# Kernel optimization log

Hardware: AMD Instinct MI355X
Metric: run time of the kernel (lower is better)

The kernel has to match this reference:

```python
import jax, jax.numpy as jnp
import numpy as np

HEADS = 16
DIM_HEAD = 64


def setup_inputs() -> dict:
    key = jax.random.key(0)
    k1, k2, k3 = jax.random.split(key, 3)
    b, n, dim = 4, 2048, 1024
    inner = HEADS * DIM_HEAD  # 1024
    x = jax.random.normal(k1, (b, n, dim), dtype=jnp.float32)
    # Dense weights, scaled like Glorot-ish init to keep softmax well-behaved
    w_qkv = jax.random.normal(k2, (dim, 3 * inner), dtype=jnp.float32) * (dim ** -0.5)
    w_out = jax.random.normal(k3, (inner, dim), dtype=jnp.float32) * (inner ** -0.5)
    b_out = jnp.zeros((dim,), dtype=jnp.float32)
    return {"x": x, "w_qkv": w_qkv, "w_out": w_out, "b_out": b_out}


def reference(x, w_qkv, w_out, b_out):
    b, n, dim = x.shape
    scale = DIM_HEAD ** -0.5
    qkv = x @ w_qkv  # [b, n, 3*h*d]
    q, k, v = jnp.split(qkv, 3, axis=-1)
    # 'b n (h d) -> b h n d'
    split_heads = lambda t: t.reshape(b, n, HEADS, DIM_HEAD).transpose(0, 2, 1, 3)
    q, k, v = split_heads(q), split_heads(k), split_heads(v)
    sim = jnp.einsum('bhid,bhjd->bhij', q, k) * scale  # [b, h, n, n]
    attn = jax.nn.softmax(sim, axis=-1)
    out = jnp.einsum('bhij,bhjd->bhid', attn, v)  # [b, h, n, d]
    out = out.transpose(0, 2, 1, 3).reshape(b, n, HEADS * DIM_HEAD)
    return out @ w_out + b_out  # dropout rate 0.0 -> identity
```

## Files before the change

### kernel.cpp

```cpp
#include <hip/hip_runtime.h>
#include <cstdint>

#define HEADS 16
#define DH 64
#define SEQ 2048
#define BATCH 4
#define DIM 1024
#define MTOT (BATCH*SEQ)
#define NQKV (3*DIM)

typedef short bf16x8 __attribute__((ext_vector_type(8)));
typedef float f32x4 __attribute__((ext_vector_type(4)));
typedef float f32x16 __attribute__((ext_vector_type(16)));

__device__ __forceinline__ unsigned short f2bf(float f) {
  union { float fv; unsigned int u; } c; c.fv = f;
  unsigned int u = c.u;
  u += 0x7FFFu + ((u >> 16) & 1u);
  return (unsigned short)(u >> 16);
}

__device__ __forceinline__ unsigned int cvtpk(float lo, float hi) {
  unsigned int r;
  asm("v_cvt_pk_bf16_f32 %0, %1, %2" : "=v"(r) : "v"(lo), "v"(hi));
  return r;
}

__device__ __forceinline__ f32x4 mfma16(bf16x8 a, bf16x8 b, f32x4 c) {
  return __builtin_amdgcn_mfma_f32_16x16x32_bf16(a, b, c, 0, 0, 0);
}
__device__ __forceinline__ f32x16 mfma32(bf16x8 a, bf16x8 b, f32x16 c) {
  return __builtin_amdgcn_mfma_f32_32x32x16_bf16(a, b, c, 0, 0, 0);
}

typedef const __attribute__((address_space(1))) unsigned int* gas_ptr;
typedef __attribute__((address_space(3))) unsigned int* las_ptr;
__device__ __forceinline__ void gl2lds16(const void* g, void* l) {
  __builtin_amdgcn_global_load_lds((gas_ptr)g, (las_ptr)l, 16, 0, 0);
}

#define QSCALE 0.18033688011112042f

__global__ __launch_bounds__(256) void cast_f32_bf16(
    const float* __restrict__ in, unsigned short* __restrict__ out, int n4) {
  int i = blockIdx.x * blockDim.x + threadIdx.x;
  if (i >= n4) return;
  float4 v = reinterpret_cast<const float4*>(in)[i];
  uint2 o;
  o.x = (unsigned int)f2bf(v.x) | ((unsigned int)f2bf(v.y) << 16);
  o.y = (unsigned int)f2bf(v.z) | ((unsigned int)f2bf(v.w) << 16);
  reinterpret_cast<uint2*>(out)[i] = o;
}

__global__ __launch_bounds__(256) void transpose_cast(
    const float* __restrict__ in, unsigned short* __restrict__ out, int R, int C) {
  __shared__ float tile[32][33];
  int c0 = blockIdx.x * 32, r0 = blockIdx.y * 32;
  int tx = threadIdx.x & 31, ty = threadIdx.x >> 5;
  for (int i = 0; i < 32; i += 8)
    tile[ty + i][tx] = in[(size_t)(r0 + ty + i) * C + c0 + tx];
  __syncthreads();
  for (int i = 0; i < 32; i += 8)
    out[(size_t)(c0 + ty + i) * R + r0 + tx] = f2bf(tile[tx][ty + i]);
}

__global__ __launch_bounds__(256) void transpose_v(
    const unsigned short* __restrict__ V, unsigned short* __restrict__ Vt) {
  __shared__ unsigned short tile[64][72];
  int n0 = blockIdx.x * 64;
  size_t base = (size_t)blockIdx.y * SEQ * DH;
  int t = threadIdx.x;
  int r = t >> 2, c = (t & 3) * 8;
  *(uint4*)&tile[r][c]      = *(const uint4*)&V[base + (size_t)(n0 + r) * DH + c];
  *(uint4*)&tile[r][c + 32] = *(const uint4*)&V[base + (size_t)(n0 + r) * DH + c + 32];
  __syncthreads();
#pragma unroll
  for (int p = 0; p < 2; p++) {
    alignas(16) unsigned short tmp[8];
#pragma unroll
    for (int i = 0; i < 8; i++) tmp[i] = tile[c + p * 32 + i][r];
    *(uint4*)&Vt[base + (size_t)r * SEQ + n0 + c + p * 32] = *(uint4*)tmp;
  }
}

#define BM 128
#define BN 128
#define BK 32
#define LDT 32

__global__ __launch_bounds__(256) void gemm_qkv(
    const unsigned short* __restrict__ A, const unsigned short* __restrict__ Bt,
    unsigned short* __restrict__ Q, unsigned short* __restrict__ K,
    unsigned short* __restrict__ V) {
  __shared__ unsigned short sA[BM * LDT];
  __shared__ unsigned short sB[BN * LDT];
  const int KD = 1024;
  int m0 = blockIdx.y * BM;
  int n0 = blockIdx.x * BN;
  int t = threadIdx.x;
  int lane = t & 63, w = t >> 6;
  int wm = (w >> 1) * 64, wn = (w & 1) * 64;
  int fr = lane & 15, fq = (lane >> 4) * 8;

  const unsigned short* gA = &A[(size_t)(m0 + w * 16 + (lane >> 2)) * KD + (lane & 3) * 8];
  const unsigned short* gB = &Bt[(size_t)(n0 + w * 16 + (lane >> 2)) * KD + (lane & 3) * 8];
  char* lA = (char*)sA + w * 1024;
  char* lB = (char*)sB + w * 1024;

  f32x4 acc[4][4];
#pragma unroll
  for (int i = 0; i < 4; i++)
#pragma unroll
    for (int j = 0; j < 4; j++) { f32x4 z = {0.f, 0.f, 0.f, 0.f}; acc[i][j] = z; }

  for (int k0 = 0; k0 < KD; k0 += BK) {
    gl2lds16(gA + k0, lA);
    gl2lds16(gA + (size_t)64 * KD + k0, lA + 4096);
    gl2lds16(gB + k0, lB);
    gl2lds16(gB + (size_t)64 * KD + k0, lB + 4096);
    __syncthreads();
    bf16x8 af[4], bfr[4];
#pragma unroll
    for (int mt = 0; mt < 4; mt++)
      af[mt] = *reinterpret_cast<const bf16x8*>(&sA[(wm + mt * 16 + fr) * LDT + fq]);
#pragma unroll
    for (int nt = 0; nt < 4; nt++)
      bfr[nt] = *reinterpret_cast<const bf16x8*>(&sB[(wn + nt * 16 + fr) * LDT + fq]);
#pragma unroll
    for (int mt = 0; mt < 4; mt++)
#pragma unroll
      for (int nt = 0; nt < 4; nt++)
        acc[mt][nt] = mfma16(af[mt], bfr[nt], acc[mt][nt]);
    __syncthreads();
  }
  int rowq = (lane >> 4) * 4;
#pragma unroll
  for (int mt = 0; mt < 4; mt++)
#pragma unroll
    for (int nt = 0; nt < 4; nt++)
#pragma unroll
      for (int r = 0; r < 4; r++) {
        int m = m0 + wm + mt * 16 + rowq + r;
        int ncol = n0 + wn + nt * 16 + fr;
        int which = ncol >> 10;
        int hd = ncol & 1023;
        int b = m >> 11, nrow = m & 2047;
        float v = acc[mt][nt][r];
        if (which == 0) v *= QSCALE;
        unsigned short* dst = (which == 0) ? Q : (which == 1 ? K : V);
        size_t idx = ((size_t)(b * HEADS + (hd >> 6)) * SEQ + nrow) * DH + (hd & 63);
        dst[idx] = f2bf(v);
      }
}

__global__ __launch_bounds__(256) void gemm_out(
    const unsigned short* __restrict__ A, const unsigned short* __restrict__ Bt,
    const float* __restrict__ bias, float* __restrict__ C) {
  __shared__ unsigned short sA[BM * LDT];
  __shared__ unsigned short sB[BN * LDT];
  const int KD = 1024;
  int m0 = blockIdx.y * BM;
  int n0 = blockIdx.x * BN;
  int t = threadIdx.x;
  int lane = t & 63, w = t >> 6;
  int wm = (w >> 1) * 64, wn = (w & 1) * 64;
  int fr = lane & 15, fq = (lane >> 4) * 8;

  const unsigned short* gA = &A[(size_t)(m0 + w * 16 + (lane >> 2)) * KD + (lane & 3) * 8];
  const unsigned short* gB = &Bt[(size_t)(n0 + w * 16 + (lane >> 2)) * KD + (lane & 3) * 8];
  char* lA = (char*)sA + w * 1024;
  char* lB = (char*)sB + w * 1024;

  f32x4 acc[4][4];
#pragma unroll
  for (int i = 0; i < 4; i++)
#pragma unroll
    for (int j = 0; j < 4; j++) { f32x4 z = {0.f, 0.f, 0.f, 0.f}; acc[i][j] = z; }

  for (int k0 = 0; k0 < KD; k0 += BK) {
    gl2lds16(gA + k0, lA);
    gl2lds16(gA + (size_t)64 * KD + k0, lA + 4096);
    gl2lds16(gB + k0, lB);
    gl2lds16(gB + (size_t)64 * KD + k0, lB + 4096);
    __syncthreads();
    bf16x8 af[4], bfr[4];
#pragma unroll
    for (int mt = 0; mt < 4; mt++)
      af[mt] = *reinterpret_cast<const bf16x8*>(&sA[(wm + mt * 16 + fr) * LDT + fq]);
#pragma unroll
    for (int nt = 0; nt < 4; nt++)
      bfr[nt] = *reinterpret_cast<const bf16x8*>(&sB[(wn + nt * 16 + fr) * LDT + fq]);
#pragma unroll
    for (int mt = 0; mt < 4; mt++)
#pragma unroll
      for (int nt = 0; nt < 4; nt++)
        acc[mt][nt] = mfma16(af[mt], bfr[nt], acc[mt][nt]);
    __syncthreads();
  }
  int rowq = (lane >> 4) * 4;
#pragma unroll
  for (int mt = 0; mt < 4; mt++)
#pragma unroll
    for (int nt = 0; nt < 4; nt++)
#pragma unroll
      for (int r = 0; r < 4; r++) {
        int m = m0 + wm + mt * 16 + rowq + r;
        int ncol = n0 + wn + nt * 16 + fr;
        C[(size_t)m * DIM + ncol] = acc[mt][nt][r] + bias[ncol];
      }
}

#define LDA 68

__global__ __launch_bounds__(256, 4) void attention(
    const unsigned short* __restrict__ Qg, const unsigned short* __restrict__ Kg,
    const unsigned short* __restrict__ Vtg, unsigned short* __restrict__ Og) {
  __shared__ unsigned short smem[2 * 64 * 72];
  unsigned short* sK  = smem;
  unsigned short* sVt = smem + 64 * LDA;

  int gid = blockIdx.x + 16 * (blockIdx.y + 16 * blockIdx.z);
  int qb   = (gid >> 3) & 15;
  int pair = ((gid & 7) << 3) | (gid >> 7);
  int h = pair & 15, b = pair >> 4;

  size_t base = (size_t)(b * HEADS + h) * SEQ * DH;
  const unsigned short* Q = Qg + base;
  const unsigned short* K = Kg + base;
  const unsigned short* Vt = Vtg + base;
  int t = threadIdx.x, lane = t & 63, w = t >> 6;
  int m = lane & 31, kh = lane >> 5;
  int q0 = qb * 128 + w * 32;

  bf16x8 qf[4];
#pragma unroll
  for (int kt = 0; kt < 4; kt++)
    qf[kt] = *reinterpret_cast<const bf16x8*>(
        &Q[(size_t)(q0 + m) * DH + kt * 16 + kh * 8]);

  f32x16 oaccT[2];
#pragma unroll
  for (int dh = 0; dh < 2; dh++)
#pragma unroll
    for (int i = 0; i < 16; i++) oaccT[dh][i] = 0.f;
  float rs = 0.f;

  int sr = t >> 2, sc = (t & 3) * 8;

  for (int j0 = 0; j0 < SEQ; j0 += 64) {
    {
      uint4 a0 = *(const uint4*)&K[(size_t)(j0 + sr) * DH + sc];
      uint4 a1 = *(const uint4*)&K[(size_t)(j0 + sr) * DH + sc + 32];
      uint4 b0 = *(const uint4*)&Vt[(size_t)sr * SEQ + j0 + sc];
      uint4 b1 = *(const uint4*)&Vt[(size_t)sr * SEQ + j0 + sc + 32];
      unsigned short* pk0 = &sK[sr * LDA + sc];
      unsigned short* pk1 = &sK[sr * LDA + sc + 32];
      unsigned short* pv0 = &sVt[sr * LDA + sc];
      unsigned short* pv1 = &sVt[sr * LDA + sc + 32];
      *(uint2*)pk0       = make_uint2(a0.x, a0.y);
      *(uint2*)(pk0 + 4) = make_uint2(a0.z, a0.w);
      *(uint2*)pk1       = make_uint2(a1.x, a1.y);
      *(uint2*)(pk1 + 4) = make_uint2(a1.z, a1.w);
      *(uint2*)pv0       = make_uint2(b0.x, b0.y);
      *(uint2*)(pv0 + 4) = make_uint2(b0.z, b0.w);
      *(uint2*)pv1       = make_uint2(b1.x, b1.y);
      *(uint2*)(pv1 + 4) = make_uint2(b1.z, b1.w);
    }
    __syncthreads();

    unsigned int pp[8][2];
#pragma unroll
    for (int jt = 0; jt < 2; jt++) {
      bf16x8 kf[4];
#pragma unroll
      for (int kt = 0; kt < 4; kt++) {
        union { uint2 u[2]; bf16x8 v; } kc;
        const unsigned short* p = &sK[(jt * 32 + m) * LDA + (2 * kt + kh) * 8];
        kc.u[0] = *(const uint2*)p;
        kc.u[1] = *(const uint2*)(p + 4);
        kf[kt] = kc.v;
      }
      f32x16 s;
#pragma unroll
      for (int i = 0; i < 16; i++) s[i] = 0.f;
#pragma unroll
      for (int kt = 0; kt < 4; kt++)
        s = mfma32(kf[kt], qf[kt], s);
      float e[16];
#pragma unroll
      for (int i = 0; i < 16; i++) e[i] = __builtin_amdgcn_exp2f(s[i]);
      float t0 = (e[0] + e[1]) + (e[2] + e[3]);
      float t1 = (e[4] + e[5]) + (e[6] + e[7]);
      float t2 = (e[8] + e[9]) + (e[10] + e[11]);
      float t3 = (e[12] + e[13]) + (e[14] + e[15]);
      rs += (t0 + t1) + (t2 + t3);
#pragma unroll
      for (int sl = 0; sl < 4; sl++) {
        pp[4 * jt + sl][0] = cvtpk(e[4 * sl + 0], e[4 * sl + 1]);
        pp[4 * jt + sl][1] = cvtpk(e[4 * sl + 2], e[4 * sl + 3]);
      }
    }

#pragma unroll
    for (int kb = 0; kb < 4; kb++) {
#pragma unroll
      for (int dh = 0; dh < 2; dh++) {
        union { uint2 u[2]; bf16x8 v; } ac;
        const unsigned short* p = &sVt[(32 * dh + m) * LDA + 16 * kb + 4 * kh];
        ac.u[0] = *(const uint2*)p;
        ac.u[1] = *(const uint2*)(p + 8);
        union { unsigned int u[4]; bf16x8 v; } bc;
        bc.u[0] = pp[2 * kb][0];
        bc.u[1] = pp[2 * kb][1];
        bc.u[2] = pp[2 * kb + 1][0];
        bc.u[3] = pp[2 * kb + 1][1];
        oaccT[dh] = mfma32(ac.v, bc.v, oaccT[dh]);
      }
    }
    __syncthreads();
  }

  float inv;
  {
    float tot = rs + __shfl_xor(rs, 32);
    inv = 1.0f / tot;
  }

  unsigned int* ew = (unsigned int*)smem + (size_t)w * 32 * 36;
#pragma unroll
  for (int dh = 0; dh < 2; dh++)
#pragma unroll
    for (int sl = 0; sl < 4; sl++) {
      unsigned int u0 = cvtpk(oaccT[dh][4 * sl + 0] * inv, oaccT[dh][4 * sl + 1] * inv);
      unsigned int u1 = cvtpk(oaccT[dh][4 * sl + 2] * inv, oaccT[dh][4 * sl + 3] * inv);
      uint2 pk; pk.x = u0; pk.y = u1;
      *(uint2*)&ew[m * 36 + 16 * dh + 4 * sl + 2 * kh] = pk;
    }
  {
    int mr = lane >> 3, ch = lane & 7;
#pragma unroll
    for (int it = 0; it < 4; it++) {
      uint4 vv = *(const uint4*)&ew[(8 * it + mr) * 36 + ch * 4];
      int n = q0 + 8 * it + mr;
      *(uint4*)&Og[((size_t)(b * SEQ + n)) * DIM + h * DH + ch * 8] = vv;
    }
  }
}

extern "C" void kernel_launch(void* const* d_in, const int* in_sizes, int n_in,
                              void* d_out, int out_size, void* d_ws, size_t ws_size,
                              hipStream_t stream) {
  const float* x     = (const float*)d_in[0];
  const float* w_qkv = (const float*)d_in[1];
  const float* w_out = (const float*)d_in[2];
  const float* b_out = (const float*)d_in[3];
  float* out = (float*)d_out;

  char* ws = (char*)d_ws;
  unsigned short* xb     = (unsigned short*)ws; ws += (size_t)MTOT * DIM * 2;
  unsigned short* wqkv_t = (unsigned short*)ws; ws += (size_t)NQKV * DIM * 2;
  unsigned short* wout_t = (unsigned short*)ws; ws += (size_t)DIM * DIM * 2;
  unsigned short* qb_    = (unsigned short*)ws; ws += (size_t)BATCH * HEADS * SEQ * DH * 2;
  unsigned short* kb_    = (unsigned short*)ws; ws += (size_t)BATCH * HEADS * SEQ * DH * 2;
  unsigned short* vb_    = (unsigned short*)ws; ws += (size_t)BATCH * HEADS * SEQ * DH * 2;
  unsigned short* attnb  = (unsigned short*)ws; ws += (size_t)MTOT * DIM * 2;
  unsigned short* vt_    = xb;

  cast_f32_bf16<<<(MTOT * DIM / 4 + 255) / 256, 256, 0, stream>>>(x, xb, MTOT * DIM / 4);
  transpose_cast<<<dim3(NQKV / 32, DIM / 32), 256, 0, stream>>>(w_qkv, wqkv_t, DIM, NQKV);
  transpose_cast<<<dim3(DIM / 32, DIM / 32), 256, 0, stream>>>(w_out, wout_t, DIM, DIM);

  gemm_qkv<<<dim3(NQKV / BN, MTOT / BM), 256, 0, stream>>>(xb, wqkv_t, qb_, kb_, vb_);

  transpose_v<<<dim3(SEQ / 64, BATCH * HEADS), 256, 0, stream>>>(vb_, vt_);

  attention<<<dim3(SEQ / 128, HEADS, BATCH), 256, 0, stream>>>(qb_, kb_, vt_, attnb);

  gemm_out<<<dim3(DIM / BN, MTOT / BM), 256, 0, stream>>>(attnb, wout_t, b_out, out);
}
```

Measured before the change: 269.5 us.

## Double-buffer K/V tiles in attention with register prefetch and swizzle GEMM tile order

The attention kernel now keeps two LDS buffers for K and V^T and prefetches the next 64-key tile into registers while computing on the current one, so global load latency is hidden behind MFMA work. The loop is unrolled by two with one barrier per tile instead of two, and the MFMA sections are wrapped in s_setprio to favour matrix issue. Both GEMMs remap block IDs with a swizzle so that consecutive blocks share rows and columns of the operands, improving L2 reuse. The cost is doubled LDS per attention block, which could lower occupancy under the 4-blocks-per-CU bound, plus extra registers for the prefetch.

Result: slower. 418.3 us (+55.2%).

```diff
diff --git a/kernel.cpp b/kernel.cpp
--- a/kernel.cpp
+++ b/kernel.cpp
@@ -95,8 +95,10 @@
   __shared__ unsigned short sA[BM * LDT];
   __shared__ unsigned short sB[BN * LDT];
   const int KD = 1024;
-  int m0 = blockIdx.y * BM;
-  int n0 = blockIdx.x * BN;
+  int gid = blockIdx.x + 24 * blockIdx.y;
+  int swz = (gid & 7) * 192 + (gid >> 3);
+  int m0 = (swz / 24) * BM;
+  int n0 = (swz % 24) * BN;
   int t = threadIdx.x;
   int lane = t & 63, w = t >> 6;
   int wm = (w >> 1) * 64, wn = (w & 1) * 64;
@@ -159,8 +161,10 @@
   __shared__ unsigned short sA[BM * LDT];
   __shared__ unsigned short sB[BN * LDT];
   const int KD = 1024;
-  int m0 = blockIdx.y * BM;
-  int n0 = blockIdx.x * BN;
+  int gid = blockIdx.x + 8 * blockIdx.y;
+  int swz = (gid & 7) * 64 + (gid >> 3);
+  int m0 = (swz / 8) * BM;
+  int n0 = (swz % 8) * BN;
   int t = threadIdx.x;
   int lane = t & 63, w = t >> 6;
   int wm = (w >> 1) * 64, wn = (w & 1) * 64;
@@ -215,9 +219,11 @@
 __global__ __launch_bounds__(256, 4) void attention(
     const unsigned short* __restrict__ Qg, const unsigned short* __restrict__ Kg,
     const unsigned short* __restrict__ Vtg, unsigned short* __restrict__ Og) {
-  __shared__ unsigned short smem[2 * 64 * 72];
-  unsigned short* sK  = smem;
-  unsigned short* sVt = smem + 64 * LDA;
+  __shared__ unsigned short smem[4 * 64 * LDA];
+  unsigned short* sK0  = smem;
+  unsigned short* sVt0 = smem + 64 * LDA;
+  unsigned short* sK1  = smem + 2 * 64 * LDA;
+  unsigned short* sVt1 = smem + 3 * 64 * LDA;
 
   int gid = blockIdx.x + 16 * (blockIdx.y + 16 * blockIdx.z);
   int qb   = (gid >> 3) & 15;
@@ -245,29 +251,29 @@
     for (int i = 0; i < 16; i++) oaccT[dh][i] = 0.f;
   float rs = 0.f;
 
-  int sr = t >> 2, sc = (t & 3) * 8;
-
-  for (int j0 = 0; j0 < SEQ; j0 += 64) {
-    {
-      uint4 a0 = *(const uint4*)&K[(size_t)(j0 + sr) * DH + sc];
-      uint4 a1 = *(const uint4*)&K[(size_t)(j0 + sr) * DH + sc + 32];
-      uint4 b0 = *(const uint4*)&Vt[(size_t)sr * SEQ + j0 + sc];
-      uint4 b1 = *(const uint4*)&Vt[(size_t)sr * SEQ + j0 + sc + 32];
-      unsigned short* pk0 = &sK[sr * LDA + sc];
-      unsigned short* pk1 = &sK[sr * LDA + sc + 32];
-      unsigned short* pv0 = &sVt[sr * LDA + sc];
-      unsigned short* pv1 = &sVt[sr * LDA + sc + 32];
-      *(uint2*)pk0       = make_uint2(a0.x, a0.y);
-      *(uint2*)(pk0 + 4) = make_uint2(a0.z, a0.w);
-      *(uint2*)pk1       = make_uint2(a1.x, a1.y);
-      *(uint2*)(pk1 + 4) = make_uint2(a1.z, a1.w);
-      *(uint2*)pv0       = make_uint2(b0.x, b0.y);
-      *(uint2*)(pv0 + 4) = make_uint2(b0.z, b0.w);
-      *(uint2*)pv1       = make_uint2(b1.x, b1.y);
-      *(uint2*)(pv1 + 4) = make_uint2(b1.z, b1.w);
-    }
-    __syncthreads();
-
+  int srow = ((t >> 1) & 31) | ((t >> 7) << 5);
+  int sch  = ((t & 1) | (((t >> 6) & 1) << 1)) * 8;
+  const unsigned short* gK = &K[(size_t)srow * DH + sch];
+  const unsigned short* gV = &Vt[(size_t)srow * SEQ + sch];
+  int ldst = srow * LDA + sch;
+
+  uint4 rka, rkb, rva, rvb;
+
+#define STAGE_LOAD(J0) { \
+    rka = *(const uint4*)&gK[(size_t)(J0) * DH]; \
+    rkb = *(const uint4*)&gK[(size_t)(J0) * DH + 32]; \
+    rva = *(const uint4*)&gV[(J0)]; \
+    rvb = *(const uint4*)&gV[(J0) + 32]; }
+
+#define W16(P, V4) { \
+    *(uint2*)(P)       = make_uint2((V4).x, (V4).y); \
+    *(uint2*)((P) + 4) = make_uint2((V4).z, (V4).w); }
+
+#define STAGE_WRITE(SK, SV) { \
+    W16(&(SK)[ldst], rka); W16(&(SK)[ldst + 32], rkb); \
+    W16(&(SV)[ldst], rva); W16(&(SV)[ldst + 32], rvb); }
+
+  auto compute = [&](const unsigned short* sKp, const unsigned short* sVp) {
     unsigned int pp[8][2];
 #pragma unroll
     for (int jt = 0; jt < 2; jt++) {
@@ -275,7 +281,7 @@
 #pragma unroll
       for (int kt = 0; kt < 4; kt++) {
         union { uint2 u[2]; bf16x8 v; } kc;
-        const unsigned short* p = &sK[(jt * 32 + m) * LDA + (2 * kt + kh) * 8];
+        const unsigned short* p = &sKp[(jt * 32 + m) * LDA + (2 * kt + kh) * 8];
         kc.u[0] = *(const uint2*)p;
         kc.u[1] = *(const uint2*)(p + 4);
         kf[kt] = kc.v;
@@ -283,9 +289,11 @@
       f32x16 s;
 #pragma unroll
       for (int i = 0; i < 16; i++) s[i] = 0.f;
+      __builtin_amdgcn_s_setprio(1);
 #pragma unroll
       for (int kt = 0; kt < 4; kt++)
         s = mfma32(kf[kt], qf[kt], s);
+      __builtin_amdgcn_s_setprio(0);
       float e[16];
 #pragma unroll
       for (int i = 0; i < 16; i++) e[i] = __builtin_amdgcn_exp2f(s[i]);
@@ -300,13 +308,13 @@
         pp[4 * jt + sl][1] = cvtpk(e[4 * sl + 2], e[4 * sl + 3]);
       }
     }
-
+    __builtin_amdgcn_s_setprio(1);
 #pragma unroll
     for (int kb = 0; kb < 4; kb++) {
 #pragma unroll
       for (int dh = 0; dh < 2; dh++) {
         union { uint2 u[2]; bf16x8 v; } ac;
-        const unsigned short* p = &sVt[(32 * dh + m) * LDA + 16 * kb + 4 * kh];
+        const unsigned short* p = &sVp[(32 * dh + m) * LDA + 16 * kb + 4 * kh];
         ac.u[0] = *(const uint2*)p;
         ac.u[1] = *(const uint2*)(p + 8);
         union { unsigned int u[4]; bf16x8 v; } bc;
@@ -317,8 +325,24 @@
         oaccT[dh] = mfma32(ac.v, bc.v, oaccT[dh]);
       }
     }
-    __syncthreads();
-  }
+    __builtin_amdgcn_s_setprio(0);
+  };
+
+  STAGE_LOAD(0);
+  STAGE_WRITE(sK0, sVt0);
+
+#pragma unroll 1
+  for (int t0 = 0; t0 < SEQ; t0 += 128) {
+    __syncthreads();
+    STAGE_LOAD(t0 + 64);
+    compute(sK0, sVt0);
+    STAGE_WRITE(sK1, sVt1);
+    __syncthreads();
+    if (t0 + 128 < SEQ) STAGE_LOAD(t0 + 128);
+    compute(sK1, sVt1);
+    if (t0 + 128 < SEQ) STAGE_WRITE(sK0, sVt0);
+  }
+  __syncthreads();
 
   float inv;
   {
@@ -345,6 +369,9 @@
       *(uint4*)&Og[((size_t)(b * SEQ + n)) * DIM + h * DH + ch * 8] = vv;
     }
   }
+#undef STAGE_LOAD
+#undef STAGE_WRITE
+#undef W16
 }
 
 extern "C" void kernel_launch(void* const* d_in, const int* in_sizes, int n_in,
```
